# Performance work log

Hardware: AMD Instinct MI355X
Metric: run time of the kernel (lower is better)

Reference implementation:

```python
import math
import jax, jax.numpy as jnp
import numpy as np

SIGMA_S = 2.0
SIGMA_R = 0.1
KERNEL_SIZE = 9
PAD = KERNEL_SIZE // 2
_COORDS = list(range(-PAD, PAD + 1))
OFFSETS = [(i, j) for i in _COORDS for j in _COORDS]
SPATIAL_W = [math.exp(-((i * i + j * j) / (2.0 * SIGMA_S ** 2))) for i, j in OFFSETS]

B, C, H, W = 16, 1, 768, 1024


def setup_inputs() -> dict:
    key = jax.random.key(0)
    k1, k2, k3 = jax.random.split(key, 3)
    depth = jax.random.uniform(k1, (B, C, H, W), dtype=jnp.float32)
    vals = jax.random.uniform(k2, (B, C, H, W), dtype=jnp.float32)
    mask = jax.random.uniform(k3, (B, C, H, W)) < 0.05
    sparse = jnp.where(mask, vals, jnp.float32(1.0))
    return {"sparse": sparse, "depth": depth}


def reference(sparse, depth):
    pad = PAD
    # sparse padded with the 'missing' sentinel 1.0; depth reflect-padded
    sp = jnp.pad(sparse, ((0, 0), (0, 0), (pad, pad), (pad, pad)), mode="constant", constant_values=1.0)
    dp = jnp.pad(depth, ((0, 0), (0, 0), (pad, pad), (pad, pad)), mode="reflect")
    num = jnp.zeros_like(sparse)
    den = jnp.zeros_like(sparse)
    inv_two_sr2 = 1.0 / (2.0 * SIGMA_R ** 2)
    Hh, Ww = sparse.shape[-2], sparse.shape[-1]
    for (dy, dx), w in zip(OFFSETS, SPATIAL_W):
        sp_shift = sp[..., pad + dy : pad + dy + Hh, pad + dx : pad + dx + Ww]
        dp_shift = dp[..., pad + dy : pad + dy + Hh, pad + dx : pad + dx + Ww]
        valid = (sp_shift != 1.0).astype(sparse.dtype)
        diff = dp_shift - depth
        range_w = jnp.exp(-(diff * diff) * inv_two_sr2)
        w_total = w * range_w * valid
        num = num + w_total * sp_shift
        den = den + w_total
    out = num / (den + 1e-8)
    out = jnp.where(den < 1e-8, jnp.ones_like(out), out)
    return out
```

## Files before the change

kernel.cpp:

```cpp
#include <hip/hip_runtime.h>


#define HH 768
#define WW 1024
#define BB 16

#define COEF_S (-0.18033688011112042f)
#define COEF_R (-72.13475204444817f)

__device__ __forceinline__ int rfl(int x) {
    return __builtin_amdgcn_readfirstlane(x);
}
__device__ __forceinline__ float rlanef(float v, int b) {
    return __int_as_float(__builtin_amdgcn_readlane(__float_as_int(v), b));
}

__device__ __forceinline__ void entry_body(
    int b, int k, float svk, float dvk,
    int px0, int py0, float fgy, float fgx, float myd,
    float& num, float& den)
{
    const float sv_b = rlanef(svk, b);
    const float dv_b = rlanef(dvk, b);
    const float eyf = (float)(py0 + (b >> 2));
    const float exf = (float)(px0 + k + ((b & 3) << 2));
    const float dy = eyf - fgy;
    const float dx = exf - fgx;
    const float r2 = fmaf(dy, dy, dx * dx);
    const bool inbox = fmaxf(fabsf(dy), fabsf(dx)) < 4.5f;
    const float diff = dv_b - myd;
    const float arg = fmaf(diff, diff * COEF_R, r2 * COEF_S);
    float w = __builtin_amdgcn_exp2f(arg);
    w = inbox ? w : 0.0f;
    num = fmaf(w, sv_b, num);
    den += w;
}

__global__ __launch_bounds__(256) void jbf_kernel(
    const float* __restrict__ sparse,
    const float* __restrict__ depth,
    float* __restrict__ out)
{
    const int tid  = (int)threadIdx.x;
    const int lane = tid & 63;
    const int wv   = tid >> 6;
    const int tx = rfl(((int)blockIdx.x << 4) + ((wv & 1) << 3));
    const int ty = rfl(((int)blockIdx.y << 4) + ((wv >> 1) << 3));
    const int px0 = rfl(min(max(tx - 4, 0), WW - 16));
    const int py0 = rfl(min(max(ty - 4, 0), HH - 16));

    const size_t plane = (size_t)blockIdx.z * (size_t)(HH * WW);
    const float* sp = sparse + plane;
    const float* dp = depth  + plane;

    const int ry  = lane >> 2;
    const int rxg = (lane & 3) << 2;
    const int woff = (py0 + ry) * WW + (px0 + rxg);
    const float4 s4 = *(const float4*)(sp + woff);
    const float4 d4 = *(const float4*)(dp + woff);

    const int my = lane >> 3, mx = lane & 7;
    const int gy = ty + my,  gx = tx + mx;
    const float myd = dp[gy * WW + gx];
    const float fgy = (float)gy, fgx = (float)gx;

    float numA = 0.0f, denA = 0.0f, numB = 0.0f, denB = 0.0f;

    #pragma unroll
    for (int k = 0; k < 4; ++k) {
        const float svk = (k == 0) ? s4.x : (k == 1) ? s4.y : (k == 2) ? s4.z : s4.w;
        const float dvk = (k == 0) ? d4.x : (k == 1) ? d4.y : (k == 2) ? d4.z : d4.w;
        unsigned long long m = __ballot(svk != 1.0f);
        while (m) {
            const int b0 = (int)__builtin_ctzll(m);
            m &= (m - 1ull);
            entry_body(b0, k, svk, dvk, px0, py0, fgy, fgx, myd, numA, denA);
            if (m) {
                const int b1 = (int)__builtin_ctzll(m);
                m &= (m - 1ull);
                entry_body(b1, k, svk, dvk, px0, py0, fgy, fgx, myd, numB, denB);
            }
        }
    }

    const float num = numA + numB;
    const float den = denA + denB;
    float res = num * __builtin_amdgcn_rcpf(den + 1e-8f);
    res = (den < 1e-8f) ? 1.0f : res;
    out[plane + (size_t)(gy * WW + gx)] = res;
}

extern "C" void kernel_launch(void* const* d_in, const int* in_sizes, int n_in,
                              void* d_out, int out_size, void* d_ws, size_t ws_size,
                              hipStream_t stream)
{
    const float* sparse = (const float*)d_in[0];
    const float* depth  = (const float*)d_in[1];
    float* out = (float*)d_out;
    dim3 grid(WW / 16, HH / 16, BB);
    jbf_kernel<<<grid, dim3(256, 1, 1), 0, stream>>>(sparse, depth, out);
}
```

Before: 194.2 us.

## Use LDS spatial-weight table and two outputs per lane with packed math

Each wave now computes a 16x8 output tile, two pixels per lane, over a 24-wide window, which halves the grid. Spatial weights and the out-of-box mask come from a shared-memory lookup table padded with -1e30, replacing the per-entry distance and box-test arithmetic. Two-wide vector math is used for the accumulation. The cost is an LDS table init with two barriers per block and extra LDS reads per sparse entry.

New measurement: 176.0 us. -9.4%, faster.

```diff
diff --git a/kernel.cpp b/kernel.cpp
--- a/kernel.cpp
+++ b/kernel.cpp
@@ -4,90 +4,132 @@
 #define HH 768
 #define WW 1024
 #define BB 16
+#define CS (-0.18033688011112042f)
+#define CR (-72.13475204444817f)
 
-#define COEF_S (-0.18033688011112042f)
-#define COEF_R (-72.13475204444817f)
+#define TS 48
+#define TROWS 31
+#define TSIZE (TROWS * TS)
 
-__device__ __forceinline__ int rfl(int x) {
-    return __builtin_amdgcn_readfirstlane(x);
-}
+typedef float f2 __attribute__((ext_vector_type(2)));
+
+__device__ __forceinline__ int rfl(int x) { return __builtin_amdgcn_readfirstlane(x); }
 __device__ __forceinline__ float rlanef(float v, int b) {
     return __int_as_float(__builtin_amdgcn_readlane(__float_as_int(v), b));
 }
-
-__device__ __forceinline__ void entry_body(
-    int b, int k, float svk, float dvk,
-    int px0, int py0, float fgy, float fgx, float myd,
-    float& num, float& den)
-{
-    const float sv_b = rlanef(svk, b);
-    const float dv_b = rlanef(dvk, b);
-    const float eyf = (float)(py0 + (b >> 2));
-    const float exf = (float)(px0 + k + ((b & 3) << 2));
-    const float dy = eyf - fgy;
-    const float dx = exf - fgx;
-    const float r2 = fmaf(dy, dy, dx * dx);
-    const bool inbox = fmaxf(fabsf(dy), fabsf(dx)) < 4.5f;
-    const float diff = dv_b - myd;
-    const float arg = fmaf(diff, diff * COEF_R, r2 * COEF_S);
-    float w = __builtin_amdgcn_exp2f(arg);
-    w = inbox ? w : 0.0f;
-    num = fmaf(w, sv_b, num);
-    den += w;
-}
+__device__ __forceinline__ f2 splat(float x) { f2 r; r.x = x; r.y = x; return r; }
 
 __global__ __launch_bounds__(256) void jbf_kernel(
     const float* __restrict__ sparse,
     const float* __restrict__ depth,
     float* __restrict__ out)
 {
+    __shared__ float Tab[TSIZE];
     const int tid  = (int)threadIdx.x;
     const int lane = tid & 63;
     const int wv   = tid >> 6;
-    const int tx = rfl(((int)blockIdx.x << 4) + ((wv & 1) << 3));
+
+    for (int i = tid; i < TSIZE; i += 256) Tab[i] = -1e30f;
+    __syncthreads();
+    if (tid < 81) {
+        const int rr = (tid * 57) >> 9;
+        const int cc = tid - 9 * rr;
+        const float dy = (float)(rr - 4), dx = (float)(cc - 4);
+        Tab[(rr + 11) * TS + cc + 19] = CS * fmaf(dy, dy, dx * dx);
+    }
+    __syncthreads();
+
+    const int tx = rfl(((int)blockIdx.x << 5) + ((wv & 1) << 4));
     const int ty = rfl(((int)blockIdx.y << 4) + ((wv >> 1) << 3));
-    const int px0 = rfl(min(max(tx - 4, 0), WW - 16));
+    const int px0 = rfl(min(max(tx - 4, 0), WW - 24));
     const int py0 = rfl(min(max(ty - 4, 0), HH - 16));
+    const int txoff = tx - px0;
+    const int tyoff = ty - py0;
 
     const size_t plane = (size_t)blockIdx.z * (size_t)(HH * WW);
     const float* sp = sparse + plane;
     const float* dp = depth  + plane;
 
-    const int ry  = lane >> 2;
-    const int rxg = (lane & 3) << 2;
-    const int woff = (py0 + ry) * WW + (px0 + rxg);
-    const float4 s4 = *(const float4*)(sp + woff);
-    const float4 d4 = *(const float4*)(dp + woff);
+    const int r  = lane >> 2;
+    const int c0 = (lane & 3) << 1;
+    const float* wbs = sp + (py0 + r) * WW + px0 + c0;
+    const float* wbd = dp + (py0 + r) * WW + px0 + c0;
+    const f2 s20 = *(const f2*)(wbs);
+    const f2 s21 = *(const f2*)(wbs + 8);
+    const f2 s22 = *(const f2*)(wbs + 16);
+    const f2 d20 = *(const f2*)(wbd);
+    const f2 d21 = *(const f2*)(wbd + 8);
+    const f2 d22 = *(const f2*)(wbd + 16);
 
     const int my = lane >> 3, mx = lane & 7;
-    const int gy = ty + my,  gx = tx + mx;
-    const float myd = dp[gy * WW + gx];
-    const float fgy = (float)gy, fgx = (float)gx;
+    const int gy = ty + my, gx = tx + mx;
+    const float myd0 = dp[gy * WW + gx];
+    const float myd1 = dp[gy * WW + gx + 8];
+    f2 nmyd; nmyd.x = -myd0; nmyd.y = -myd1;
+    const int clane_w = my * TS + mx;
 
-    float numA = 0.0f, denA = 0.0f, numB = 0.0f, denB = 0.0f;
+    f2 numA = splat(0.0f), denA = splat(0.0f);
+    f2 numB = splat(0.0f), denB = splat(0.0f);
+    const f2 crp = splat(CR);
+
+    const int sbase0 = TS * (15 - tyoff) + (23 - txoff) - 8;
 
     #pragma unroll
-    for (int k = 0; k < 4; ++k) {
-        const float svk = (k == 0) ? s4.x : (k == 1) ? s4.y : (k == 2) ? s4.z : s4.w;
-        const float dvk = (k == 0) ? d4.x : (k == 1) ? d4.y : (k == 2) ? d4.z : d4.w;
-        unsigned long long m = __ballot(svk != 1.0f);
-        while (m) {
-            const int b0 = (int)__builtin_ctzll(m);
-            m &= (m - 1ull);
-            entry_body(b0, k, svk, dvk, px0, py0, fgy, fgx, myd, numA, denA);
-            if (m) {
-                const int b1 = (int)__builtin_ctzll(m);
+    for (int j = 0; j < 3; ++j) {
+        const f2 s2 = (j == 0) ? s20 : (j == 1) ? s21 : s22;
+        const f2 d2 = (j == 0) ? d20 : (j == 1) ? d21 : d22;
+        #pragma unroll
+        for (int k = 0; k < 2; ++k) {
+            const float svk = k ? s2.y : s2.x;
+            const float dvk = k ? d2.y : d2.x;
+            const int sbase = sbase0 + 8 * j + k;
+            unsigned long long m = __ballot(svk != 1.0f);
+            while (m) {
+                const int b0 = (int)__builtin_ctzll(m);
                 m &= (m - 1ull);
-                entry_body(b1, k, svk, dvk, px0, py0, fgy, fgx, myd, numB, denB);
+                {
+                    const float sv_e = rlanef(svk, b0);
+                    const float dv_e = rlanef(dvk, b0);
+                    const int SW = sbase + (b0 >> 2) * TS + ((b0 & 3) << 1);
+                    const float* tb = Tab + (SW - clane_w);
+                    f2 tp; tp.x = tb[8]; tp.y = tb[0];
+                    const f2 diff = nmyd + splat(dv_e);
+                    const f2 q = diff * crp;
+                    const f2 arg = q * diff + tp;
+                    f2 w; w.x = __builtin_amdgcn_exp2f(arg.x);
+                    w.y = __builtin_amdgcn_exp2f(arg.y);
+                    denA += w;
+                    numA += w * splat(sv_e);
+                }
+                if (m) {
+                    const int b1 = (int)__builtin_ctzll(m);
+                    m &= (m - 1ull);
+                    const float sv_e = rlanef(svk, b1);
+                    const float dv_e = rlanef(dvk, b1);
+                    const int SW = sbase + (b1 >> 2) * TS + ((b1 & 3) << 1);
+                    const float* tb = Tab + (SW - clane_w);
+                    f2 tp; tp.x = tb[8]; tp.y = tb[0];
+                    const f2 diff = nmyd + splat(dv_e);
+                    const f2 q = diff * crp;
+                    const f2 arg = q * diff + tp;
+                    f2 w; w.x = __builtin_amdgcn_exp2f(arg.x);
+                    w.y = __builtin_amdgcn_exp2f(arg.y);
+                    denB += w;
+                    numB += w * splat(sv_e);
+                }
             }
         }
     }
 
-    const float num = numA + numB;
-    const float den = denA + denB;
-    float res = num * __builtin_amdgcn_rcpf(den + 1e-8f);
-    res = (den < 1e-8f) ? 1.0f : res;
-    out[plane + (size_t)(gy * WW + gx)] = res;
+    const float n0 = numA.x + numB.x, n1 = numA.y + numB.y;
+    const float e0 = denA.x + denB.x, e1 = denA.y + denB.y;
+    float r0 = n0 * __builtin_amdgcn_rcpf(e0 + 1e-8f);
+    r0 = (e0 < 1e-8f) ? 1.0f : r0;
+    float r1 = n1 * __builtin_amdgcn_rcpf(e1 + 1e-8f);
+    r1 = (e1 < 1e-8f) ? 1.0f : r1;
+    float* op = out + plane + (size_t)gy * WW + gx;
+    op[0] = r0;
+    op[8] = r1;
 }
 
 extern "C" void kernel_launch(void* const* d_in, const int* in_sizes, int n_in,
@@ -97,6 +139,6 @@
     const float* sparse = (const float*)d_in[0];
     const float* depth  = (const float*)d_in[1];
     float* out = (float*)d_out;
-    dim3 grid(WW / 16, HH / 16, BB);
+    dim3 grid(WW / 32, HH / 16, BB);
     jbf_kernel<<<grid, dim3(256, 1, 1), 0, stream>>>(sparse, depth, out);
 }
```
